# Optimization experiments

Hardware: AMD Instinct MI355X
Metric: run time of the kernel (lower is better)

## Reference

```python
import jax, jax.numpy as jnp
import numpy as np

NUM_HEADS = 12

def setup_inputs() -> dict:
    key = jax.random.key(0)
    k1, k2, k3, k4 = jax.random.split(key, 4)
    B, N, C = 64, 197, 768
    x = jax.random.normal(k1, (B, N, C), dtype=jnp.float32)
    w_qkv = jax.random.normal(k2, (3 * C, C), dtype=jnp.float32) * (C ** -0.5)
    w_proj = jax.random.normal(k3, (C, C), dtype=jnp.float32) * (C ** -0.5)
    b_proj = jax.random.normal(k4, (C,), dtype=jnp.float32) * 0.01
    return {"x": x, "w_qkv": w_qkv, "w_proj": w_proj, "b_proj": b_proj}

def reference(x, w_qkv, w_proj, b_proj):
    B, N, C = x.shape
    H = NUM_HEADS
    hd = C // H
    scale = hd ** -0.5
    # qkv linear (no bias): [B,N,3C] -> [3,B,H,N,hd]
    qkv = jnp.einsum('bnc,dc->bnd', x, w_qkv).reshape(B, N, 3, H, hd)
    qkv = jnp.transpose(qkv, (2, 0, 3, 1, 4))
    q, k, v = qkv[0], qkv[1], qkv[2]
    # full attention matrix [B,H,N,N] (materialized, matching the original)
    attn = jax.nn.softmax(jnp.einsum('bhnd,bhmd->bhnm', q, k) * scale, axis=-1)
    # CLS-token attention stats: mean over heads of attn row 0 (patch tokens) -> [B, N-1]
    global_attn = jnp.mean(attn[:, :, 0, 1:], axis=1)
    out = jnp.einsum('bhnm,bhmd->bhnd', attn, v)          # [B,H,N,hd]
    out = jnp.transpose(out, (0, 2, 1, 3)).reshape(B, N, C)
    out = jnp.einsum('bnc,dc->bnd', out, w_proj) + b_proj
    return out, global_attn
```

## Files before the change

kernel.cpp:

```cpp
#include <hip/hip_runtime.h>
#include <math.h>

#define B_   64
#define N_   197
#define C_   768
#define H_   12
#define HD_  64
#define BH_  (B_ * H_)
#define M_   (B_ * N_)

typedef _Float16 half8 __attribute__((ext_vector_type(8)));
typedef float    f32x4 __attribute__((ext_vector_type(4)));

#define XH_OFF   0u
#define WQH_OFF  19365888u
#define WPH_OFF  22904832u
#define QH_OFF   24084480u
#define KH_OFF   43450368u
#define VH_OFF   62816256u
#define OH_OFF   82182144u
#define P0_OFF   101548032u
#define WS_BYTES 102150144u

__device__ __forceinline__ half8 h8zero() {
    half8 z;
    #pragma unroll
    for (int i = 0; i < 8; ++i) z[i] = (_Float16)0;
    return z;
}

__device__ __forceinline__ void async16(const _Float16* g, _Float16* l) {
    __builtin_amdgcn_global_load_lds(
        (const __attribute__((address_space(1))) void*)g,
        (__attribute__((address_space(3))) void*)l,
        16, 0, 0);
}

__device__ __forceinline__ int xcd_swz(int i, int nwg) {
    const int q = nwg >> 3, r = nwg & 7;
    const int xcd = i & 7, j = i >> 3;
    return (xcd < r ? xcd * (q + 1) : r * (q + 1) + (xcd - r) * q) + j;
}

__global__ void k_ws_too_small(float* out, float ws_bytes) { out[0] = -ws_bytes; }

__global__ __launch_bounds__(256) void k_cvt_all(const float* __restrict__ x,
                                                 const float* __restrict__ wq,
                                                 const float* __restrict__ wp,
                                                 _Float16* __restrict__ Xh,
                                                 _Float16* __restrict__ Wqh,
                                                 _Float16* __restrict__ Wph) {
    int i = blockIdx.x * blockDim.x + threadIdx.x;
    const float* src;
    _Float16*    dst;
    if (i < 1210368)      { src = x;  dst = Xh; }
    else if (i < 1431552) { src = wq; dst = Wqh; i -= 1210368; }
    else                  { src = wp; dst = Wph; i -= 1431552; }
    float4 f0 = *(const float4*)(src + (size_t)i * 8);
    float4 f1 = *(const float4*)(src + (size_t)i * 8 + 4);
    half8 h;
    h[0]=(_Float16)f0.x; h[1]=(_Float16)f0.y; h[2]=(_Float16)f0.z; h[3]=(_Float16)f0.w;
    h[4]=(_Float16)f1.x; h[5]=(_Float16)f1.y; h[6]=(_Float16)f1.z; h[7]=(_Float16)f1.w;
    *(half8*)(dst + (size_t)i * 8) = h;
}

__device__ __forceinline__ void mfma_nt_core_256(const _Float16* __restrict__ A,
                                                 const _Float16* __restrict__ B,
                                                 int M, int K, int m0, int n0,
                                                 _Float16* As, _Float16* Bs,
                                                 f32x4 (&acc)[8][4]) {
    const int tid  = threadIdx.x;
    const int lane = tid & 63;
    const int w    = tid >> 6;
    const int wm   = w >> 2, wn = w & 3;
    const int ln   = lane & 15, kq = lane >> 4;

    const int srow = tid >> 3;
    const int kcs  = (((tid & 7) ^ (srow & 7)) << 3);
    int ra00 = m0 +       srow; if (ra00 >= M) ra00 = 0;
    int ra01 = m0 +  64 + srow; if (ra01 >= M) ra01 = 0;
    int ra10 = m0 + 128 + srow; if (ra10 >= M) ra10 = 0;
    int ra11 = m0 + 192 + srow; if (ra11 >= M) ra11 = 0;
    const _Float16* A00 = A + (size_t)ra00 * K + kcs;
    const _Float16* A01 = A + (size_t)ra01 * K + kcs;
    const _Float16* A10 = A + (size_t)ra10 * K + kcs;
    const _Float16* A11 = A + (size_t)ra11 * K + kcs;
    const _Float16* B00 = B + (size_t)(n0 +       srow) * K + kcs;
    const _Float16* B01 = B + (size_t)(n0 +  64 + srow) * K + kcs;
    const _Float16* B10 = B + (size_t)(n0 + 128 + srow) * K + kcs;
    const _Float16* B11 = B + (size_t)(n0 + 192 + srow) * K + kcs;
    const int dOff = w << 9;

    const int kx    = (ln & 7) << 3;
    const int aBase = wm * 8192 + ln * 64;
    const int bBase = (wn >> 1) * 8192 + (wn & 1) * 4096 + ln * 64;

    half8 af[4][2], bf[4][2];

    async16(A00, As + dOff);          async16(A01, As + 4096 + dOff);
    async16(A10, As + 8192 + dOff);   async16(A11, As + 12288 + dOff);
    async16(B00, Bs + dOff);          async16(B01, Bs + 4096 + dOff);
    async16(B10, Bs + 8192 + dOff);   async16(B11, Bs + 12288 + dOff);

    const int NT = K >> 6;
    #pragma unroll 1
    for (int t = 0; t < NT; ++t) {
        const int cur  = (t & 1) << 14;
        const int nb   = 16384 - cur;
        const int koff = (t + 1) << 6;
        const bool pre = (t + 1 < NT);
        const _Float16* Ac = As + cur;
        const _Float16* Bc = Bs + cur;

        if (pre) {
            async16(A00 + koff, As + nb + dOff);
            async16(A01 + koff, As + nb + 4096 + dOff);
            async16(A10 + koff, As + nb + 8192 + dOff);
            async16(A11 + koff, As + nb + 12288 + dOff);
            asm volatile("s_waitcnt vmcnt(4)" ::: "memory");
        } else {
            asm volatile("s_waitcnt vmcnt(0)" ::: "memory");
        }
        __builtin_amdgcn_s_barrier();
        __builtin_amdgcn_sched_barrier(0);
        #pragma unroll
        for (int m4 = 0; m4 < 4; ++m4)
            #pragma unroll
            for (int kk = 0; kk < 2; ++kk)
                af[m4][kk] = *(const half8*)&Ac[aBase + m4 * 1024 + ((kk * 32 + kq * 8) ^ kx)];
        #pragma unroll
        for (int n2 = 0; n2 < 2; ++n2)
            #pragma unroll
            for (int kk = 0; kk < 2; ++kk)
                bf[n2][kk] = *(const half8*)&Bc[bBase + n2 * 1024 + ((kk * 32 + kq * 8) ^ kx)];
        __builtin_amdgcn_s_setprio(1);
        #pragma unroll
        for (int m4 = 0; m4 < 4; ++m4)
            #pragma unroll
            for (int n2 = 0; n2 < 2; ++n2)
                #pragma unroll
                for (int kk = 0; kk < 2; ++kk)
                    acc[m4][n2] = __builtin_amdgcn_mfma_f32_16x16x32_f16(af[m4][kk], bf[n2][kk], acc[m4][n2], 0, 0, 0);
        __builtin_amdgcn_s_setprio(0);
        __builtin_amdgcn_sched_barrier(0);
        __builtin_amdgcn_s_barrier();

        if (pre) {
            async16(B00 + koff, Bs + nb + dOff);
            async16(B01 + koff, Bs + nb + 4096 + dOff);
        }
        #pragma unroll
        for (int n2 = 0; n2 < 2; ++n2)
            #pragma unroll
            for (int kk = 0; kk < 2; ++kk)
                bf[2 + n2][kk] = *(const half8*)&Bc[bBase + (2 + n2) * 1024 + ((kk * 32 + kq * 8) ^ kx)];
        __builtin_amdgcn_s_setprio(1);
        #pragma unroll
        for (int m4 = 0; m4 < 4; ++m4)
            #pragma unroll
            for (int n2 = 0; n2 < 2; ++n2)
                #pragma unroll
                for (int kk = 0; kk < 2; ++kk)
                    acc[m4][2 + n2] = __builtin_amdgcn_mfma_f32_16x16x32_f16(af[m4][kk], bf[2 + n2][kk], acc[m4][2 + n2], 0, 0, 0);
        __builtin_amdgcn_s_setprio(0);
        __builtin_amdgcn_sched_barrier(0);
        __builtin_amdgcn_s_barrier();

        if (pre) {
            async16(B10 + koff, Bs + nb + 8192 + dOff);
            async16(B11 + koff, Bs + nb + 12288 + dOff);
        }
        #pragma unroll
        for (int m4 = 0; m4 < 4; ++m4)
            #pragma unroll
            for (int kk = 0; kk < 2; ++kk)
                af[m4][kk] = *(const half8*)&Ac[aBase + (4 + m4) * 1024 + ((kk * 32 + kq * 8) ^ kx)];
        __builtin_amdgcn_s_setprio(1);
        #pragma unroll
        for (int m4 = 0; m4 < 4; ++m4)
            #pragma unroll
            for (int n2 = 0; n2 < 2; ++n2)
                #pragma unroll
                for (int kk = 0; kk < 2; ++kk)
                    acc[4 + m4][n2] = __builtin_amdgcn_mfma_f32_16x16x32_f16(af[m4][kk], bf[n2][kk], acc[4 + m4][n2], 0, 0, 0);
        __builtin_amdgcn_s_setprio(0);
        __builtin_amdgcn_sched_barrier(0);
        __builtin_amdgcn_s_barrier();

        __builtin_amdgcn_s_setprio(1);
        #pragma unroll
        for (int m4 = 0; m4 < 4; ++m4)
            #pragma unroll
            for (int n2 = 0; n2 < 2; ++n2)
                #pragma unroll
                for (int kk = 0; kk < 2; ++kk)
                    acc[4 + m4][2 + n2] = __builtin_amdgcn_mfma_f32_16x16x32_f16(af[m4][kk], bf[2 + n2][kk], acc[4 + m4][2 + n2], 0, 0, 0);
        __builtin_amdgcn_s_setprio(0);
        asm volatile("s_waitcnt lgkmcnt(0)" ::: "memory");
        __builtin_amdgcn_sched_barrier(0);
        __builtin_amdgcn_s_barrier();
    }
}

__device__ __forceinline__ void mfma_nt_core_h(const _Float16* __restrict__ A,
                                               const _Float16* __restrict__ B,
                                               int M, int K, int m0, int n0,
                                               _Float16* As, _Float16* Bs,
                                               f32x4 (&acc)[4][4]) {
    const int tid  = threadIdx.x;
    const int wave = tid >> 6, lane = tid & 63;
    const int wr   = (wave >> 1) << 6;
    const int wc   = (wave & 1) << 6;
    const int ln   = lane & 15, kq = lane >> 4;

    const int row0 = tid >> 2;
    const int ch0  = (tid & 3) << 3;
    int ar0 = m0 + row0;        if (ar0 >= M) ar0 = 0;
    int ar1 = m0 + 64 + row0;   if (ar1 >= M) ar1 = 0;
    const _Float16* A0 = A + (size_t)ar0 * K + ch0;
    const _Float16* A1 = A + (size_t)ar1 * K + ch0;
    const _Float16* B0 = B + (size_t)(n0 + row0) * K + ch0;
    const _Float16* B1 = B + (size_t)(n0 + 64 + row0) * K + ch0;
    _Float16* AsD = As + (wave << 9);
    _Float16* BsD = Bs + (wave << 9);

    async16(A0, AsD);        async16(A1, AsD + 2048);
    async16(B0, BsD);        async16(B1, BsD + 2048);
    __syncthreads();

    int cur = 0;
    for (int k0 = 0; k0 < K; k0 += 32) {
        const int nxt = cur ^ 1;
        if (k0 + 32 < K) {
            const int nb = nxt << 12;
            async16(A0 + k0 + 32, AsD + nb);
            async16(A1 + k0 + 32, AsD + nb + 2048);
            async16(B0 + k0 + 32, BsD + nb);
            async16(B1 + k0 + 32, BsD + nb + 2048);
        }
        const _Float16* Ac = As + (cur << 12);
        const _Float16* Bc = Bs + (cur << 12);
        half8 af[4], bf[4];
        #pragma unroll
        for (int t = 0; t < 4; ++t) {
            af[t] = *(const half8*)&Ac[(wr + t * 16 + ln) * 32 + kq * 8];
            bf[t] = *(const half8*)&Bc[(wc + t * 16 + ln) * 32 + kq * 8];
        }
        #pragma unroll
        for (int i = 0; i < 4; ++i)
            #pragma unroll
            for (int j = 0; j < 4; ++j)
                acc[i][j] = __builtin_amdgcn_mfma_f32_16x16x32_f16(af[i], bf[j], acc[i][j], 0, 0, 0);
        __syncthreads();
        cur = nxt;
    }
}

__global__ __launch_bounds__(512, 2) void k_qkv_mfma(const _Float16* __restrict__ Xh,
                                                     const _Float16* __restrict__ Wq,
                                                     _Float16* __restrict__ Qh,
                                                     _Float16* __restrict__ Kh,
                                                     _Float16* __restrict__ Vh) {
    __shared__ _Float16 As[32768];
    __shared__ _Float16 Bs[32768];
    const int work = xcd_swz(blockIdx.x, 50 * 9);
    const int m0 = (work / 9) << 8;
    const int n0 = (work % 9) << 8;
    f32x4 acc[8][4] = {};
    mfma_nt_core_256(Xh, Wq, M_, C_, m0, n0, As, Bs, acc);

    const int lane = threadIdx.x & 63;
    const int w    = threadIdx.x >> 6;
    const int wm = w >> 2, wn = w & 3;
    const int ln = lane & 15, kq = lane >> 4;

    _Float16* basep[4];
    float     scl[4];
    #pragma unroll
    for (int ni = 0; ni < 4; ++ni) {
        const int d  = n0 + wn * 64 + ni * 16 + ln;
        const int t3 = d / C_;
        const int rr = d - t3 * C_;
        const int h  = rr >> 6;
        const int e  = rr & 63;
        _Float16* tp = (t3 == 0) ? Qh : (t3 == 1) ? Kh : Vh;
        basep[ni] = tp + (size_t)h * N_ * HD_ + e;
        scl[ni]   = (t3 == 0) ? 0.125f : 1.f;
    }
    #pragma unroll
    for (int mi = 0; mi < 8; ++mi) {
        #pragma unroll
        for (int i = 0; i < 4; ++i) {
            const int m = m0 + wm * 128 + mi * 16 + kq * 4 + i;
            if (m >= M_) continue;
            const int b = m / N_;
            const int n = m - b * N_;
            const size_t rowoff = ((size_t)b * H_ * N_ + n) * HD_;
            #pragma unroll
            for (int ni = 0; ni < 4; ++ni)
                basep[ni][rowoff] = (_Float16)(acc[mi][ni][i] * scl[ni]);
        }
    }
}

__global__ __launch_bounds__(256) void k_proj_mfma(const _Float16* __restrict__ Oh,
                                                   const _Float16* __restrict__ Wp,
                                                   const float* __restrict__ bias,
                                                   float* __restrict__ out) {
    __shared__ _Float16 As[2 * 4096];
    __shared__ _Float16 Bs[2 * 4096];
    const int work = xcd_swz(blockIdx.y * 6 + blockIdx.x, 6 * 99);
    const int m0 = (work / 6) << 7;
    const int n0 = (work % 6) << 7;
    f32x4 acc[4][4] = {};
    mfma_nt_core_h(Oh, Wp, M_, C_, m0, n0, As, Bs, acc);

    const int lane = threadIdx.x & 63;
    const int wave = threadIdx.x >> 6;
    const int wr = (wave >> 1) << 6, wc = (wave & 1) << 6;
    const int ln = lane & 15, kq = lane >> 4;
    float bv[4];
    #pragma unroll
    for (int nt = 0; nt < 4; ++nt) bv[nt] = bias[n0 + wc + nt * 16 + ln];
    #pragma unroll
    for (int mt = 0; mt < 4; ++mt) {
        #pragma unroll
        for (int i = 0; i < 4; ++i) {
            const int m = m0 + wr + mt * 16 + kq * 4 + i;
            if (m >= M_) continue;
            #pragma unroll
            for (int nt = 0; nt < 4; ++nt)
                out[(size_t)m * C_ + n0 + wc + nt * 16 + ln] = acc[mt][nt][i] + bv[nt];
        }
    }
}

__global__ __launch_bounds__(256) void k_attn(const _Float16* __restrict__ Qh,
                                              const _Float16* __restrict__ Kh,
                                              const _Float16* __restrict__ Vh,
                                              _Float16* __restrict__ Oh,
                                              float* __restrict__ P0) {
    __shared__ _Float16 lds[39936];
    _Float16* Ks = lds;
    _Float16* Vt = lds + 13312;
    _Float16* Pl = lds + 26624;

    const int bh = blockIdx.x;
    const int b = bh / H_, h = bh - b * H_;
    const int tid = threadIdx.x, wave = tid >> 6, lane = tid & 63;
    const int ln = lane & 15, kq = lane >> 4;
    const size_t kvb = (size_t)bh * N_ * HD_;

    for (int idx = tid; idx < 208 * 8; idx += 256) {
        const int key = idx >> 3, c8 = idx & 7;
        half8 v = (key < N_) ? *(const half8*)(Kh + kvb + (size_t)key * HD_ + c8 * 8) : h8zero();
        *(half8*)&Ks[key * 64 + ((c8 ^ (key & 7)) << 3)] = v;
    }
    for (int idx = tid; idx < 197 * 8; idx += 256) {
        const int key = idx >> 3, c = (idx & 7) << 3;
        half8 v = *(const half8*)(Vh + kvb + (size_t)key * HD_ + c);
        #pragma unroll
        for (int j = 0; j < 8; ++j) Vt[(c + j) * 208 + key] = v[j];
    }
    for (int idx = tid; idx < 64 * 11; idx += 256) {
        const int d = idx / 11, k = 197 + (idx - d * 11);
        Vt[d * 208 + k] = (_Float16)0;
    }
    __syncthreads();

    _Float16* Pw = Pl + wave * 16 * 208;
    const int swz = ln & 7;

    for (int rt = 0; rt < 4; ++rt) {
        if (rt * 64 + wave * 16 >= N_) continue;

        const int qrow = rt * 64 + wave * 16 + ln;
        const _Float16* Qp = Qh + kvb + (size_t)((qrow < N_) ? qrow : 0) * HD_ + kq * 8;
        half8 qf0 = *(const half8*)Qp;
        half8 qf1 = *(const half8*)(Qp + 32);

        f32x4 acc[13] = {};
        __builtin_amdgcn_s_setprio(1);
        #pragma unroll
        for (int c = 0; c < 13; ++c) {
            const _Float16* kp = &Ks[(c * 16 + ln) * 64];
            half8 kf0 = *(const half8*)(kp + ((kq ^ swz) << 3));
            half8 kf1 = *(const half8*)(kp + (((4 + kq) ^ swz) << 3));
            acc[c] = __builtin_amdgcn_mfma_f32_16x16x32_f16(qf0, kf0, acc[c], 0, 0, 0);
            acc[c] = __builtin_amdgcn_mfma_f32_16x16x32_f16(qf1, kf1, acc[c], 0, 0, 0);
        }
        __builtin_amdgcn_s_setprio(0);

        float inv4[4];
        #pragma unroll
        for (int r = 0; r < 4; ++r) {
            float m = -1e30f;
            #pragma unroll
            for (int c = 0; c < 13; ++c) {
                float x = ((c * 16 + ln) < N_) ? acc[c][r] : -1e30f;
                acc[c][r] = x;
                m = fmaxf(m, x);
            }
            m = fmaxf(m, __shfl_xor(m, 1)); m = fmaxf(m, __shfl_xor(m, 2));
            m = fmaxf(m, __shfl_xor(m, 4)); m = fmaxf(m, __shfl_xor(m, 8));
            float s = 0.f;
            #pragma unroll
            for (int c = 0; c < 13; ++c) { float e = __expf(acc[c][r] - m); acc[c][r] = e; s += e; }
            s += __shfl_xor(s, 1); s += __shfl_xor(s, 2);
            s += __shfl_xor(s, 4); s += __shfl_xor(s, 8);
            inv4[r] = 1.f / s;
        }

        #pragma unroll
        for (int c = 0; c < 13; ++c) {
            const int col = c * 16 + ln;
            #pragma unroll
            for (int r = 0; r < 4; ++r)
                Pw[(kq * 4 + r) * 208 + col] = (_Float16)(acc[c][r] * inv4[r]);
        }

        if (rt == 0 && wave == 0 && kq == 0) {
            #pragma unroll
            for (int c = 0; c < 13; ++c) {
                const int col = c * 16 + ln;
                if (col >= 1 && col < N_) P0[(size_t)bh * 196 + col - 1] = acc[c][0] * inv4[0];
            }
        }
        asm volatile("s_waitcnt lgkmcnt(0)" ::: "memory");
        __builtin_amdgcn_sched_barrier(0);

        f32x4 o4[4] = {};
        __builtin_amdgcn_s_setprio(1);
        #pragma unroll
        for (int t = 0; t < 6; ++t) {
            half8 pf = *(const half8*)&Pw[ln * 208 + kq * 8 + 32 * t];
            #pragma unroll
            for (int n = 0; n < 4; ++n) {
                half8 vf = *(const half8*)&Vt[(n * 16 + ln) * 208 + kq * 8 + 32 * t];
                o4[n] = __builtin_amdgcn_mfma_f32_16x16x32_f16(pf, vf, o4[n], 0, 0, 0);
            }
        }
        {
            const int off6 = (kq < 2) ? (192 + kq * 8) : 0;
            half8 pf = *(const half8*)&Pw[ln * 208 + off6];
            if (kq >= 2) pf = h8zero();
            #pragma unroll
            for (int n = 0; n < 4; ++n) {
                half8 vf = *(const half8*)&Vt[(n * 16 + ln) * 208 + off6];
                o4[n] = __builtin_amdgcn_mfma_f32_16x16x32_f16(pf, vf, o4[n], 0, 0, 0);
            }
        }
        __builtin_amdgcn_s_setprio(0);

        const int g0 = rt * 64 + wave * 16 + kq * 4;
        #pragma unroll
        for (int r = 0; r < 4; ++r) {
            const int g = g0 + r;
            if (g >= N_) continue;
            _Float16* op = Oh + ((size_t)b * N_ + g) * C_ + h * HD_;
            #pragma unroll
            for (int n = 0; n < 4; ++n) op[n * 16 + ln] = (_Float16)o4[n][r];
        }
    }
}

__global__ void k_gattn(const float* __restrict__ P0, float* __restrict__ out2) {
    const int idx = blockIdx.x * blockDim.x + threadIdx.x;
    const int b = idx / (N_ - 1), m = idx - b * (N_ - 1);
    float s = 0.f;
    #pragma unroll
    for (int h = 0; h < H_; ++h) s += P0[((size_t)(b * H_ + h)) * 196 + m];
    out2[idx] = s * (1.f / H_);
}

extern "C" void kernel_launch(void* const* d_in, const int* in_sizes, int n_in,
                              void* d_out, int out_size, void* d_ws, size_t ws_size,
                              hipStream_t stream) {
    const float* x      = (const float*)d_in[0];
    const float* w_qkv  = (const float*)d_in[1];
    const float* w_proj = (const float*)d_in[2];
    const float* b_proj = (const float*)d_in[3];
    float* out = (float*)d_out;
    char* ws   = (char*)d_ws;

    if (ws_size < (size_t)WS_BYTES) {
        k_ws_too_small<<<1, 1, 0, stream>>>(out, (float)ws_size);
        return;
    }

    _Float16* Xh  = (_Float16*)(ws + XH_OFF);
    _Float16* Wqh = (_Float16*)(ws + WQH_OFF);
    _Float16* Wph = (_Float16*)(ws + WPH_OFF);
    _Float16* Qh  = (_Float16*)(ws + QH_OFF);
    _Float16* Kh  = (_Float16*)(ws + KH_OFF);
    _Float16* Vh  = (_Float16*)(ws + VH_OFF);
    _Float16* Oh  = (_Float16*)(ws + OH_OFF);
    float*    P0  = (float*)   (ws + P0_OFF);

    k_cvt_all<<<5880, 256, 0, stream>>>(x, w_qkv, w_proj, Xh, Wqh, Wph);

    k_qkv_mfma <<<dim3(450),   512, 0, stream>>>(Xh, Wqh, Qh, Kh, Vh);
    k_attn     <<<dim3(BH_),   256, 0, stream>>>(Qh, Kh, Vh, Oh, P0);
    k_gattn    <<<dim3(49),    256, 0, stream>>>(P0, out + (size_t)M_ * C_);
    k_proj_mfma<<<dim3(6, 99), 256, 0, stream>>>(Oh, Wph, b_proj, out);
}
```

Measured before the change: 226.3 us.

## Keep attention probabilities in registers by transposing QK^T MFMA output

Swaps the MFMA operands so the score tile comes out transposed (keys along the lane's k-quad), which lets softmax reductions use only cross-quad shuffles. The normalized probabilities then feed the PV product directly from registers through 16x16x16 MFMAs, instead of being written to an LDS P buffer and read back. This drops the P staging area and shrinks LDS, so the kernel now requests 3 blocks per CU. The V transpose buffer is repadded to stride 216. In exchange it issues twice as many smaller MFMAs for PV, and the 16x16x16 instructions may have lower throughput.

```diff
diff --git a/kernel.cpp b/kernel.cpp
--- a/kernel.cpp
+++ b/kernel.cpp
@@ -10,6 +10,7 @@
 #define M_   (B_ * N_)
 
 typedef _Float16 half8 __attribute__((ext_vector_type(8)));
+typedef _Float16 half4 __attribute__((ext_vector_type(4)));
 typedef float    f32x4 __attribute__((ext_vector_type(4)));
 
 #define XH_OFF   0u
@@ -335,15 +336,14 @@
     }
 }
 
-__global__ __launch_bounds__(256) void k_attn(const _Float16* __restrict__ Qh,
-                                              const _Float16* __restrict__ Kh,
-                                              const _Float16* __restrict__ Vh,
-                                              _Float16* __restrict__ Oh,
-                                              float* __restrict__ P0) {
-    __shared__ _Float16 lds[39936];
+__global__ __launch_bounds__(256, 3) void k_attn(const _Float16* __restrict__ Qh,
+                                                 const _Float16* __restrict__ Kh,
+                                                 const _Float16* __restrict__ Vh,
+                                                 _Float16* __restrict__ Oh,
+                                                 float* __restrict__ P0) {
+    __shared__ _Float16 lds[27136];
     _Float16* Ks = lds;
     _Float16* Vt = lds + 13312;
-    _Float16* Pl = lds + 26624;
 
     const int bh = blockIdx.x;
     const int b = bh / H_, h = bh - b * H_;
@@ -360,15 +360,14 @@
         const int key = idx >> 3, c = (idx & 7) << 3;
         half8 v = *(const half8*)(Vh + kvb + (size_t)key * HD_ + c);
         #pragma unroll
-        for (int j = 0; j < 8; ++j) Vt[(c + j) * 208 + key] = v[j];
-    }
-    for (int idx = tid; idx < 64 * 11; idx += 256) {
-        const int d = idx / 11, k = 197 + (idx - d * 11);
-        Vt[d * 208 + k] = (_Float16)0;
+        for (int j = 0; j < 8; ++j) Vt[(c + j) * 216 + key] = v[j];
+    }
+    for (int idx = tid; idx < 64 * 19; idx += 256) {
+        const int d = idx / 19, k = 197 + (idx - d * 19);
+        Vt[d * 216 + k] = (_Float16)0;
     }
     __syncthreads();
 
-    _Float16* Pw = Pl + wave * 16 * 208;
     const int swz = ln & 7;
 
     for (int rt = 0; rt < 4; ++rt) {
@@ -386,68 +385,61 @@
             const _Float16* kp = &Ks[(c * 16 + ln) * 64];
             half8 kf0 = *(const half8*)(kp + ((kq ^ swz) << 3));
             half8 kf1 = *(const half8*)(kp + (((4 + kq) ^ swz) << 3));
-            acc[c] = __builtin_amdgcn_mfma_f32_16x16x32_f16(qf0, kf0, acc[c], 0, 0, 0);
-            acc[c] = __builtin_amdgcn_mfma_f32_16x16x32_f16(qf1, kf1, acc[c], 0, 0, 0);
-        }
-        __builtin_amdgcn_s_setprio(0);
-
-        float inv4[4];
+            acc[c] = __builtin_amdgcn_mfma_f32_16x16x32_f16(kf0, qf0, acc[c], 0, 0, 0);
+            acc[c] = __builtin_amdgcn_mfma_f32_16x16x32_f16(kf1, qf1, acc[c], 0, 0, 0);
+        }
+        __builtin_amdgcn_s_setprio(0);
+
+        float m = -1e30f;
+        #pragma unroll
+        for (int c = 0; c < 12; ++c)
+            #pragma unroll
+            for (int r = 0; r < 4; ++r) m = fmaxf(m, acc[c][r]);
         #pragma unroll
         for (int r = 0; r < 4; ++r) {
-            float m = -1e30f;
-            #pragma unroll
-            for (int c = 0; c < 13; ++c) {
-                float x = ((c * 16 + ln) < N_) ? acc[c][r] : -1e30f;
-                acc[c][r] = x;
-                m = fmaxf(m, x);
+            float x = (kq * 4 + r < 5) ? acc[12][r] : -1e30f;
+            acc[12][r] = x;
+            m = fmaxf(m, x);
+        }
+        m = fmaxf(m, __shfl_xor(m, 16));
+        m = fmaxf(m, __shfl_xor(m, 32));
+        float s = 0.f;
+        #pragma unroll
+        for (int c = 0; c < 13; ++c)
+            #pragma unroll
+            for (int r = 0; r < 4; ++r) {
+                float e = __expf(acc[c][r] - m);
+                acc[c][r] = e;
+                s += e;
             }
-            m = fmaxf(m, __shfl_xor(m, 1)); m = fmaxf(m, __shfl_xor(m, 2));
-            m = fmaxf(m, __shfl_xor(m, 4)); m = fmaxf(m, __shfl_xor(m, 8));
-            float s = 0.f;
-            #pragma unroll
-            for (int c = 0; c < 13; ++c) { float e = __expf(acc[c][r] - m); acc[c][r] = e; s += e; }
-            s += __shfl_xor(s, 1); s += __shfl_xor(s, 2);
-            s += __shfl_xor(s, 4); s += __shfl_xor(s, 8);
-            inv4[r] = 1.f / s;
-        }
-
-        #pragma unroll
-        for (int c = 0; c < 13; ++c) {
-            const int col = c * 16 + ln;
-            #pragma unroll
-            for (int r = 0; r < 4; ++r)
-                Pw[(kq * 4 + r) * 208 + col] = (_Float16)(acc[c][r] * inv4[r]);
-        }
-
-        if (rt == 0 && wave == 0 && kq == 0) {
-            #pragma unroll
-            for (int c = 0; c < 13; ++c) {
-                const int col = c * 16 + ln;
-                if (col >= 1 && col < N_) P0[(size_t)bh * 196 + col - 1] = acc[c][0] * inv4[0];
-            }
-        }
-        asm volatile("s_waitcnt lgkmcnt(0)" ::: "memory");
-        __builtin_amdgcn_sched_barrier(0);
+        s += __shfl_xor(s, 16);
+        s += __shfl_xor(s, 32);
+        const float inv = 1.f / s;
+
+        if (rt == 0 && wave == 0 && ln == 0) {
+            #pragma unroll
+            for (int c = 0; c < 13; ++c)
+                #pragma unroll
+                for (int r = 0; r < 4; ++r) {
+                    const int key = c * 16 + kq * 4 + r;
+                    if (key >= 1 && key < N_)
+                        P0[(size_t)bh * 196 + key - 1] = acc[c][r] * inv;
+                }
+        }
 
         f32x4 o4[4] = {};
         __builtin_amdgcn_s_setprio(1);
         #pragma unroll
-        for (int t = 0; t < 6; ++t) {
-            half8 pf = *(const half8*)&Pw[ln * 208 + kq * 8 + 32 * t];
+        for (int u = 0; u < 13; ++u) {
+            half4 af;
+            af[0] = (_Float16)(acc[u][0] * inv);
+            af[1] = (_Float16)(acc[u][1] * inv);
+            af[2] = (_Float16)(acc[u][2] * inv);
+            af[3] = (_Float16)(acc[u][3] * inv);
             #pragma unroll
             for (int n = 0; n < 4; ++n) {
-                half8 vf = *(const half8*)&Vt[(n * 16 + ln) * 208 + kq * 8 + 32 * t];
-                o4[n] = __builtin_amdgcn_mfma_f32_16x16x32_f16(pf, vf, o4[n], 0, 0, 0);
-            }
-        }
-        {
-            const int off6 = (kq < 2) ? (192 + kq * 8) : 0;
-            half8 pf = *(const half8*)&Pw[ln * 208 + off6];
-            if (kq >= 2) pf = h8zero();
-            #pragma unroll
-            for (int n = 0; n < 4; ++n) {
-                half8 vf = *(const half8*)&Vt[(n * 16 + ln) * 208 + off6];
-                o4[n] = __builtin_amdgcn_mfma_f32_16x16x32_f16(pf, vf, o4[n], 0, 0, 0);
+                half4 bf = *(const half4*)&Vt[(n * 16 + ln) * 216 + u * 16 + kq * 4];
+                o4[n] = __builtin_amdgcn_mfma_f32_16x16x16f16(af, bf, o4[n], 0, 0, 0);
             }
         }
         __builtin_amdgcn_s_setprio(0);
```

After: 220.6 us. 2.5% less time.
